# Kernel optimization log

Hardware: AMD Instinct MI355X
Metric: run time of the kernel (lower is better)

## Reference

```python
import jax, jax.numpy as jnp
import numpy as np

N = 16000      # points
K = 16         # neighbors per query (fixed-degree CSR)
M = N * K      # attention pairs
C = 384        # embed_dim
H = 6          # num_heads
HD = C // H    # head_dim = 64
L = 25         # quant_grid_length = window/quant = 6.0/0.24
T2 = 2 * L - 1 # rel-pos table length = 49
WIN = 6.0
QUANT = 0.24
SCALE = HD ** -0.5


def setup_inputs() -> dict:
    key = jax.random.key(0)
    ks = jax.random.split(key, 12)
    feats = jax.random.normal(ks[0], (N, C), jnp.float32)
    xyz = jax.random.uniform(ks[1], (N, 3), jnp.float32) * 240.0
    index_0 = jnp.repeat(jnp.arange(N, dtype=jnp.int32), K)            # sorted query ids per pair
    index_0_offsets = jnp.arange(0, M + 1, K, dtype=jnp.int32)         # CSR offsets
    index_1 = jax.random.randint(ks[2], (M,), 0, N, jnp.int32)         # key ids per pair
    sort_idx = jax.random.permutation(ks[3], N).astype(jnp.int32)
    lin = lambda k: jax.random.normal(k, (C, C), jnp.float32) * 0.02
    tab = lambda k: jax.random.normal(k, (T2, 3, H, HD), jnp.float32) * 0.02
    return {
        'feats': feats, 'xyz': xyz,
        'index_0': index_0, 'index_0_offsets': index_0_offsets,
        'index_1': index_1, 'sort_idx': sort_idx,
        'Wq': lin(ks[4]), 'bq': jnp.zeros((C,), jnp.float32),
        'Wk': lin(ks[5]), 'bk': jnp.zeros((C,), jnp.float32),
        'Wv': lin(ks[6]), 'bv': jnp.zeros((C,), jnp.float32),
        'Wp': lin(ks[7]), 'bp': jnp.zeros((C,), jnp.float32),
        'Tq': tab(ks[8]), 'Tk': tab(ks[9]), 'Tv': tab(ks[10]),
    }


def reference(feats, xyz, index_0, index_0_offsets, index_1, sort_idx,
              Wq, bq, Wk, bk, Wv, bv, Wp, bp, Tq, Tk, Tv):
    n = feats.shape[0]
    # QKV projections (key/value default to query feats in the module)
    q = (feats @ Wq.T + bq).reshape(n, H, HD) * SCALE
    k = (feats @ Wk.T + bk).reshape(n, H, HD)
    v = (feats @ Wv.T + bv).reshape(n, H, HD)
    # sort into contiguous-window order
    qs, ks_, vs = q[sort_idx], k[sort_idx], v[sort_idx]
    xyz_s = xyz[sort_idx]
    # quantized in-window coords (shift_win=False -> shift 0)
    xq = jnp.floor(((xyz_s - xyz_s.min(0)) % WIN) / QUANT)             # [N,3], values in [0, L-1]
    i0, i1 = index_0, index_1
    rel_idx = (xq[i0] - xq[i1]).astype(jnp.int32) + (L - 1)            # [M,3] in [0, 2L-2]
    # attention logits: q.k plus contextual relative-position terms
    attn = jnp.einsum('mhd,mhd->mh', qs[i0], ks_[i1])                  # [M,H]
    for t in range(3):
        dq = jnp.einsum('nhd,lhd->nlh', qs, Tq[:, t])                  # [N,T2,H]
        dk = jnp.einsum('nhd,lhd->nlh', ks_, Tk[:, t])
        attn = attn + dq[i0, rel_idx[:, t]] + dk[i1, rel_idx[:, t]]
    # scatter softmax over CSR segments (segments given by index_0)
    amax = jax.ops.segment_max(attn, i0, num_segments=n)
    e = jnp.exp(attn - amax[i0])
    denom = jax.ops.segment_sum(e, i0, num_segments=n)
    a = e / denom[i0]                                                  # [M,H]
    # weighted value aggregation
    x = jax.ops.segment_sum(a[:, :, None] * vs[i1], i0, num_segments=n)  # [N,H,HD]
    # relative-position value contribution, factored through table bins
    for t in range(3):
        seg2 = i0 * T2 + rel_idx[:, t]
        w = jax.ops.segment_sum(a, seg2, num_segments=n * T2).reshape(n, T2, H)
        x = x + jnp.einsum('nlh,lhd->nhd', w, Tv[:, t])
    # unsort back to input order and project
    out = jnp.zeros_like(x).at[sort_idx].set(x).reshape(n, C)
    return out @ Wp.T + bp
```

## Files before the change

### kernel.cpp

```cpp
#include <hip/hip_runtime.h>
#include <hip/hip_bf16.h>
#include <cstdint>
#include <cstddef>

#define NPTS 16000
#define KNB  16
#define CDIM 384
#define NH   6
#define HDIM 64
#define T2C  49
#define NL3T 147
#define THR  160
#define NXC  1152
#define ROWB 4224
#define QOFF  0
#define KOFF  768
#define VOFF  1536
#define DQOFF 2304
#define DKOFF 3264

static constexpr float WIN    = 6.0f;
static constexpr float QUANT  = 0.24f;
static constexpr float QSCALE = 0.125f;
static constexpr float DQS    = 8.0f;
static constexpr float DQSINV = 0.125f;

typedef __attribute__((ext_vector_type(8))) short short8;
typedef __attribute__((ext_vector_type(4))) float floatx4;
typedef __attribute__((ext_vector_type(4))) unsigned short ushort4v;

__device__ inline unsigned short f2bf(float x) {
    unsigned int u = __float_as_uint(x);
    unsigned int r = (u + 0x7fffu + ((u >> 16) & 1u)) >> 16;
    return (unsigned short)r;
}
__device__ inline float bf2f(unsigned short b) {
    return __uint_as_float(((unsigned int)b) << 16);
}
__device__ inline float f8tof(unsigned char b) {
    return __builtin_amdgcn_cvt_f32_fp8((int)b, 0);
}

__global__ void init_min_kernel(unsigned int* minbits) {
    if (threadIdx.x < 3) minbits[threadIdx.x] = 0x7f800000u;
}

__global__ void min_kernel(const float* __restrict__ xyz,
                           unsigned int* __restrict__ minbits) {
    float m0 = INFINITY, m1 = INFINITY, m2 = INFINITY;
    for (int i = blockIdx.x * blockDim.x + threadIdx.x; i < NPTS;
         i += gridDim.x * blockDim.x) {
        m0 = fminf(m0, xyz[i * 3 + 0]);
        m1 = fminf(m1, xyz[i * 3 + 1]);
        m2 = fminf(m2, xyz[i * 3 + 2]);
    }
#pragma unroll
    for (int off = 1; off < 64; off <<= 1) {
        m0 = fminf(m0, __shfl_xor(m0, off, 64));
        m1 = fminf(m1, __shfl_xor(m1, off, 64));
        m2 = fminf(m2, __shfl_xor(m2, off, 64));
    }
    if ((threadIdx.x & 63) == 0) {
        atomicMin(&minbits[0], __float_as_uint(m0));
        atomicMin(&minbits[1], __float_as_uint(m1));
        atomicMin(&minbits[2], __float_as_uint(m2));
    }
}

__global__ void xq_kernel(const float* __restrict__ xyz,
                          const int* __restrict__ sort_idx,
                          const unsigned int* __restrict__ minbits,
                          int* __restrict__ xq) {
    int n = blockIdx.x * blockDim.x + threadIdx.x;
    if (n >= NPTS) return;
    int orig = sort_idx[n];
#pragma unroll
    for (int t = 0; t < 3; ++t) {
        float mn = __uint_as_float(minbits[t]);
        float v  = xyz[orig * 3 + t] - mn;
        float md = fmodf(v, WIN);
        float q  = floorf(md / QUANT);
        xq[n * 3 + t] = (int)q;
    }
}

__global__ void relpack_kernel(const int* __restrict__ idx1,
                               const int* __restrict__ xq,
                               unsigned int* __restrict__ pairs) {
    int m = blockIdx.x * blockDim.x + threadIdx.x;
    if (m >= NPTS * KNB) return;
    int n = m >> 4;
    int key = idx1[m];
    int r0 = xq[n * 3 + 0] - xq[key * 3 + 0] + 24; r0 = min(max(r0, 0), T2C - 1);
    int r1 = xq[n * 3 + 1] - xq[key * 3 + 1] + 24; r1 = min(max(r1, 0), T2C - 1);
    int r2 = xq[n * 3 + 2] - xq[key * 3 + 2] + 24; r2 = min(max(r2, 0), T2C - 1);
    pairs[m] = (unsigned)key | ((unsigned)r0 << 14) | ((unsigned)r1 << 20) |
               ((unsigned)r2 << 26);
}

#define G0 (NPTS * CDIM / 4)
#define G1 (3 * CDIM * CDIM)
#define G2 (CDIM * CDIM)
#define G3 (NH * THR * HDIM)
#define G6 (NH * THR * HDIM)
#define G7 (NH * THR * HDIM)
#define G4 (3 * CDIM)
#define G5 (CDIM)
__global__ void prep_kernel(const float* __restrict__ feats,
                            const int* __restrict__ sortix,
                            const float* __restrict__ Wq,
                            const float* __restrict__ Wk,
                            const float* __restrict__ Wv,
                            const float* __restrict__ Wp,
                            const float* __restrict__ bq,
                            const float* __restrict__ bk,
                            const float* __restrict__ bv,
                            const float* __restrict__ bp,
                            const float* __restrict__ Tv,
                            const float* __restrict__ Tq,
                            const float* __restrict__ Tk,
                            unsigned short* __restrict__ featsbf,
                            unsigned short* __restrict__ Wall,
                            unsigned short* __restrict__ Wpbf,
                            unsigned short* __restrict__ Tvh,
                            unsigned short* __restrict__ Tqh,
                            unsigned short* __restrict__ Tkh,
                            float* __restrict__ bfull,
                            float* __restrict__ bproj) {
    int i = blockIdx.x * blockDim.x + threadIdx.x;
    if (i < G0) {
        int n  = i / (CDIM / 4);
        int c4 = (i % (CDIM / 4)) * 4;
        const float4 v = *(const float4*)&feats[(size_t)sortix[n] * CDIM + c4];
        ushort4v o;
        o.x = f2bf(v.x); o.y = f2bf(v.y); o.z = f2bf(v.z); o.w = f2bf(v.w);
        *(ushort4v*)&featsbf[(size_t)n * CDIM + c4] = o;
        return;
    }
    i -= G0;
    if (i < G1) {
        int j = i / CDIM, k = i % CDIM;
        float v = (j < 384) ? Wq[j * CDIM + k]
                : (j < 768) ? Wk[(j - 384) * CDIM + k]
                            : Wv[(j - 768) * CDIM + k];
        Wall[i] = f2bf(v);
        return;
    }
    i -= G1;
    if (i < G2) { Wpbf[i] = f2bf(Wp[i]); return; }
    i -= G2;
    if (i < G3) {
        int jr = (i / HDIM) % THR, d = i % HDIM, h = i / (THR * HDIM);
        Tvh[i] = (jr < NL3T) ? f2bf(Tv[(size_t)(jr * 6 + h) * HDIM + d])
                             : (unsigned short)0;
        return;
    }
    i -= G3;
    if (i < G6) {
        int jr = (i / HDIM) % THR, d = i % HDIM, h = i / (THR * HDIM);
        Tqh[i] = (jr < NL3T) ? f2bf(Tq[(size_t)(jr * 6 + h) * HDIM + d])
                             : (unsigned short)0;
        return;
    }
    i -= G6;
    if (i < G7) {
        int jr = (i / HDIM) % THR, d = i % HDIM, h = i / (THR * HDIM);
        Tkh[i] = (jr < NL3T) ? f2bf(Tk[(size_t)(jr * 6 + h) * HDIM + d])
                             : (unsigned short)0;
        return;
    }
    i -= G7;
    if (i < G4) {
        bfull[i] = (i < 384) ? bq[i] : (i < 768) ? bk[i - 384] : bv[i - 768];
        return;
    }
    i -= G4;
    if (i < G5) { bproj[i] = bp[i]; }
}

__global__ __launch_bounds__(256) void gemm_big(
    const unsigned short* __restrict__ Abf,
    const unsigned short* __restrict__ Wmat,
    const float* __restrict__ bias,
    int mode,
    unsigned char* __restrict__ QXb, float* __restrict__ outf) {
    __shared__ unsigned short As[128 * 64];
    __shared__ unsigned short Bs[128 * 64];
    const int tid  = threadIdx.x;
    const int lane = tid & 63;
    const int w    = tid >> 6;
    const int wm   = w >> 1, wn = w & 1;

    const int nwg  = gridDim.x * gridDim.y;
    const int orig = blockIdx.y * gridDim.x + blockIdx.x;
    const int qq   = nwg >> 3, rr = nwg & 7;
    const int xcd  = orig & 7, idx = orig >> 3;
    const int wg   = (xcd < rr ? xcd * (qq + 1) : rr * (qq + 1) + (xcd - rr) * qq) + idx;
    const int jn0  = (wg % gridDim.x) * 128;
    const int m0   = (wg / gridDim.x) * 128;

    floatx4 acc[4][4];
#pragma unroll
    for (int i = 0; i < 4; ++i)
#pragma unroll
        for (int j = 0; j < 4; ++j) acc[i][j] = (floatx4)0.0f;

    for (int kt = 0; kt < 6; ++kt) {
        const int k0 = kt * 64;
#pragma unroll
        for (int q = 0; q < 4; ++q) {
            const int s    = w * 4 + q;
            const int row  = s * 8 + (lane >> 3);
            const int col  = (lane & 7) * 8;
            const unsigned short* ga = Abf  + (size_t)(m0  + row) * CDIM + k0 + col;
            const unsigned short* gb = Wmat + (size_t)(jn0 + row) * CDIM + k0 + col;
            __builtin_amdgcn_global_load_lds(
                (const __attribute__((address_space(1))) void*)ga,
                (__attribute__((address_space(3))) void*)&As[s * 512], 16, 0, 0);
            __builtin_amdgcn_global_load_lds(
                (const __attribute__((address_space(1))) void*)gb,
                (__attribute__((address_space(3))) void*)&Bs[s * 512], 16, 0, 0);
        }
        __syncthreads();
#pragma unroll
        for (int ks = 0; ks < 2; ++ks) {
            short8 a[4], b[4];
#pragma unroll
            for (int mi = 0; mi < 4; ++mi) {
                int row = wm * 64 + mi * 16 + (lane & 15);
                a[mi] = *(const short8*)&As[row * 64 + ks * 32 + (lane >> 4) * 8];
            }
#pragma unroll
            for (int ni = 0; ni < 4; ++ni) {
                int jr = wn * 64 + ni * 16 + (lane & 15);
                b[ni] = *(const short8*)&Bs[jr * 64 + ks * 32 + (lane >> 4) * 8];
            }
#pragma unroll
            for (int mi = 0; mi < 4; ++mi)
#pragma unroll
                for (int ni = 0; ni < 4; ++ni)
                    acc[mi][ni] = __builtin_amdgcn_mfma_f32_16x16x32_bf16(
                        b[ni], a[mi], acc[mi][ni], 0, 0, 0);
        }
        __syncthreads();
    }

#pragma unroll
    for (int mi = 0; mi < 4; ++mi) {
        const int n = m0 + wm * 64 + mi * 16 + (lane & 15);
#pragma unroll
        for (int ni = 0; ni < 4; ++ni) {
            const int jjb = jn0 + wn * 64 + ni * 16 + (lane >> 4) * 4;
            const float4 b4 = *(const float4*)&bias[jjb];
            const float v0 = acc[mi][ni][0] + b4.x;
            const float v1 = acc[mi][ni][1] + b4.y;
            const float v2 = acc[mi][ni][2] + b4.z;
            const float v3 = acc[mi][ni][3] + b4.w;
            if (mode == 0) {
                const float scl = (jjb < 384) ? QSCALE : 1.0f;
                ushort4v o;
                o.x = f2bf(v0 * scl); o.y = f2bf(v1 * scl);
                o.z = f2bf(v2 * scl); o.w = f2bf(v3 * scl);
                *(ushort4v*)(QXb + (size_t)n * ROWB + jjb * 2) = o;
            } else {
                float4 o; o.x = v0; o.y = v1; o.z = v2; o.w = v3;
                *(float4*)&outf[(size_t)n * CDIM + jjb] = o;
            }
        }
    }
}

__global__ __launch_bounds__(256) void dqdk_kernel(
    const unsigned char* __restrict__ QXin,
    const unsigned short* __restrict__ Tqh,
    const unsigned short* __restrict__ Tkh,
    unsigned char* __restrict__ QXout) {
    __shared__ unsigned short As[128 * 64];
    __shared__ unsigned short Bs[THR * 64];
    const int tid  = threadIdx.x;
    const int lane = tid & 63;
    const int w    = tid >> 6;
    const int wm   = w >> 1, wn = w & 1;
    const int h    = blockIdx.y;
    const bool isk = blockIdx.z != 0;
    const int srcoff = (isk ? KOFF : QOFF) + h * 128;
    const int dstoff = (isk ? DKOFF : DQOFF) + h * THR;
    const unsigned short* T = (isk ? Tkh : Tqh) + (size_t)h * THR * HDIM;
    const int m0 = blockIdx.x * 128;

#pragma unroll
    for (int q = 0; q < 4; ++q) {
        const int s   = w * 4 + q;
        const int row = s * 8 + (lane >> 3);
        const unsigned char* ga =
            QXin + (size_t)(m0 + row) * ROWB + srcoff + (lane & 7) * 16;
        __builtin_amdgcn_global_load_lds(
            (const __attribute__((address_space(1))) void*)ga,
            (__attribute__((address_space(3))) void*)&As[s * 512], 16, 0, 0);
    }
#pragma unroll
    for (int q = 0; q < 5; ++q) {
        const int s   = w * 5 + q;
        const int row = s * 8 + (lane >> 3);
        const unsigned short* gb = T + (size_t)row * HDIM + (lane & 7) * 8;
        __builtin_amdgcn_global_load_lds(
            (const __attribute__((address_space(1))) void*)gb,
            (__attribute__((address_space(3))) void*)&Bs[s * 512], 16, 0, 0);
    }
    __syncthreads();

    floatx4 acc[4][5];
#pragma unroll
    for (int i = 0; i < 4; ++i)
#pragma unroll
        for (int j = 0; j < 5; ++j) acc[i][j] = (floatx4)0.0f;

#pragma unroll
    for (int ks = 0; ks < 2; ++ks) {
        short8 a[4], b[5];
#pragma unroll
        for (int mi = 0; mi < 4; ++mi) {
            int row = wm * 64 + mi * 16 + (lane & 15);
            a[mi] = *(const short8*)&As[row * 64 + ks * 32 + (lane >> 4) * 8];
        }
#pragma unroll
        for (int ni = 0; ni < 5; ++ni) {
            int jr = wn * 80 + ni * 16 + (lane & 15);
            b[ni] = *(const short8*)&Bs[jr * 64 + ks * 32 + (lane >> 4) * 8];
        }
#pragma unroll
        for (int mi = 0; mi < 4; ++mi)
#pragma unroll
            for (int ni = 0; ni < 5; ++ni)
                acc[mi][ni] = __builtin_amdgcn_mfma_f32_16x16x32_bf16(
                    b[ni], a[mi], acc[mi][ni], 0, 0, 0);
    }

#pragma unroll
    for (int mi = 0; mi < 4; ++mi) {
        const int n = m0 + wm * 64 + mi * 16 + (lane & 15);
#pragma unroll
        for (int ni = 0; ni < 5; ++ni) {
            const int jr0 = wn * 80 + ni * 16 + (lane >> 4) * 4;
            int u = __builtin_amdgcn_cvt_pk_fp8_f32(acc[mi][ni][0] * DQS,
                                                    acc[mi][ni][1] * DQS, 0, false);
            u = __builtin_amdgcn_cvt_pk_fp8_f32(acc[mi][ni][2] * DQS,
                                                acc[mi][ni][3] * DQS, u, true);
            *(unsigned int*)(QXout + (size_t)n * ROWB + dstoff + jr0) = (unsigned)u;
        }
    }
}

__global__ __launch_bounds__(384) void attn_kernel(
    const unsigned char* __restrict__ QXb,
    const unsigned int* __restrict__ pairs,
    const unsigned short* __restrict__ Tvh,
    const int* __restrict__ sortix,
    unsigned short* __restrict__ xb) {
    const int n    = blockIdx.x;
    const int h    = threadIdx.x >> 6;
    const int lane = threadIdx.x & 63;
    const int pp   = lane >> 4, c = lane & 15;
    const int hb   = h * THR;
    const unsigned short* Tvb = Tvh + (size_t)hb * HDIM;

    const unsigned char* qrow = QXb + (size_t)n * ROWB;
    const ushort4v q4 = *(const ushort4v*)(qrow + QOFF + h * 128 + c * 8);
    const float qx = bf2f(q4.x), qy = bf2f(q4.y), qz = bf2f(q4.z), qw = bf2f(q4.w);

    unsigned int pv[4];
#pragma unroll
    for (int g = 0; g < 4; ++g) pv[g] = pairs[n * KNB + g * 4 + pp];

    const unsigned char* krow[4];
    int j0g[4], j1g[4], j2g[4];
#pragma unroll
    for (int g = 0; g < 4; ++g) {
        krow[g] = QXb + (size_t)(pv[g] & 0x3FFFu) * ROWB;
        j0g[g]  = (int)((pv[g] >> 14) & 63u) * 3;
        j1g[g]  = (int)((pv[g] >> 20) & 63u) * 3 + 1;
        j2g[g]  = (int)(pv[g] >> 26) * 3 + 2;
    }

    float tab[4];
#pragma unroll
    for (int g = 0; g < 4; ++g) {
        tab[g] = DQSINV *
            (f8tof(qrow[DQOFF + hb + j0g[g]]) + f8tof(qrow[DQOFF + hb + j1g[g]]) +
             f8tof(qrow[DQOFF + hb + j2g[g]]) +
             f8tof(krow[g][DKOFF + hb + j0g[g]]) +
             f8tof(krow[g][DKOFF + hb + j1g[g]]) +
             f8tof(krow[g][DKOFF + hb + j2g[g]]));
    }

    float lg[4];
#pragma unroll
    for (int g = 0; g < 4; ++g) {
        const ushort4v k4 = *(const ushort4v*)(krow[g] + KOFF + h * 128 + c * 8);
        lg[g] = qx * bf2f(k4.x) + qy * bf2f(k4.y) + qz * bf2f(k4.z) + qw * bf2f(k4.w);
    }
#pragma unroll
    for (int m = 1; m <= 8; m <<= 1)
#pragma unroll
        for (int g = 0; g < 4; ++g) lg[g] += __shfl_xor(lg[g], m, 64);
#pragma unroll
    for (int g = 0; g < 4; ++g) lg[g] += tab[g];

    float mx = fmaxf(fmaxf(lg[0], lg[1]), fmaxf(lg[2], lg[3]));
    mx = fmaxf(mx, __shfl_xor(mx, 16, 64));
    mx = fmaxf(mx, __shfl_xor(mx, 32, 64));
    float e[4], s = 0.f;
#pragma unroll
    for (int g = 0; g < 4; ++g) { e[g] = expf(lg[g] - mx); s += e[g]; }
    s += __shfl_xor(s, 16, 64);
    s += __shfl_xor(s, 32, 64);
    const float inv = 1.f / s;

    float xa0 = 0.f, xa1 = 0.f, xa2 = 0.f, xa3 = 0.f;
#pragma unroll
    for (int g = 0; g < 4; ++g) {
        const float wgt = e[g] * inv;
        const ushort4v v4 = *(const ushort4v*)(krow[g] + VOFF + h * 128 + c * 8);
        const ushort4v t0 = *(const ushort4v*)&Tvb[(size_t)j0g[g] * HDIM + c * 4];
        const ushort4v t1 = *(const ushort4v*)&Tvb[(size_t)j1g[g] * HDIM + c * 4];
        const ushort4v t2 = *(const ushort4v*)&Tvb[(size_t)j2g[g] * HDIM + c * 4];
        xa0 += wgt * (bf2f(v4.x) + bf2f(t0.x) + bf2f(t1.x) + bf2f(t2.x));
        xa1 += wgt * (bf2f(v4.y) + bf2f(t0.y) + bf2f(t1.y) + bf2f(t2.y));
        xa2 += wgt * (bf2f(v4.z) + bf2f(t0.z) + bf2f(t1.z) + bf2f(t2.z));
        xa3 += wgt * (bf2f(v4.w) + bf2f(t0.w) + bf2f(t1.w) + bf2f(t2.w));
    }
#pragma unroll
    for (int m = 16; m <= 32; m <<= 1) {
        xa0 += __shfl_xor(xa0, m, 64);
        xa1 += __shfl_xor(xa1, m, 64);
        xa2 += __shfl_xor(xa2, m, 64);
        xa3 += __shfl_xor(xa3, m, 64);
    }
    if (pp == 0) {
        const int dst = sortix[n];
        ushort4v o;
        o.x = f2bf(xa0); o.y = f2bf(xa1); o.z = f2bf(xa2); o.w = f2bf(xa3);
        *(ushort4v*)&xb[(size_t)dst * CDIM + h * HDIM + c * 4] = o;
    }
}

extern "C" void kernel_launch(void* const* d_in, const int* in_sizes, int n_in,
                              void* d_out, int out_size, void* d_ws,
                              size_t ws_size, hipStream_t stream) {
    const float* feats  = (const float*)d_in[0];
    const float* xyz    = (const float*)d_in[1];
    const int*   index1 = (const int*)d_in[4];
    const int*   sortix = (const int*)d_in[5];
    const float* Wq = (const float*)d_in[6];
    const float* bq = (const float*)d_in[7];
    const float* Wk = (const float*)d_in[8];
    const float* bk = (const float*)d_in[9];
    const float* Wv = (const float*)d_in[10];
    const float* bv = (const float*)d_in[11];
    const float* Wp = (const float*)d_in[12];
    const float* bp = (const float*)d_in[13];
    const float* Tq = (const float*)d_in[14];
    const float* Tk = (const float*)d_in[15];
    const float* Tv = (const float*)d_in[16];
    float* out = (float*)d_out;

    char* ws = (char*)d_ws;
    size_t off = 0;
    auto alloc = [&](size_t bytes) -> void* {
        void* p = ws + off;
        off = (off + bytes + 255) & ~(size_t)255;
        return p;
    };
    unsigned short* featsbf = (unsigned short*)alloc((size_t)NPTS * CDIM * 2);
    unsigned short* Wall    = (unsigned short*)alloc((size_t)NXC * CDIM * 2);
    unsigned short* Wpbf    = (unsigned short*)alloc((size_t)CDIM * CDIM * 2);
    unsigned short* Tvh     = (unsigned short*)alloc((size_t)NH * THR * HDIM * 2);
    unsigned short* Tqh     = (unsigned short*)alloc((size_t)NH * THR * HDIM * 2);
    unsigned short* Tkh     = (unsigned short*)alloc((size_t)NH * THR * HDIM * 2);
    float*          bfull   = (float*)alloc((size_t)NXC * sizeof(float));
    float*          bproj   = (float*)alloc((size_t)CDIM * sizeof(float));
    unsigned char*  QXb     = (unsigned char*)alloc((size_t)NPTS * ROWB);
    unsigned int*   pairs   = (unsigned int*)alloc((size_t)NPTS * KNB * 4);
    int*            xq      = (int*)alloc((size_t)NPTS * 3 * sizeof(int));
    unsigned int*   minbits = (unsigned int*)alloc(16);
    unsigned short* xb      = featsbf;

    init_min_kernel<<<1, 64, 0, stream>>>(minbits);
    min_kernel<<<128, 256, 0, stream>>>(xyz, minbits);
    xq_kernel<<<(NPTS + 255) / 256, 256, 0, stream>>>(xyz, sortix, minbits, xq);
    relpack_kernel<<<(NPTS * KNB + 255) / 256, 256, 0, stream>>>(index1, xq, pairs);

    const int prep_total = G0 + G1 + G2 + G3 + G6 + G7 + G4 + G5;
    prep_kernel<<<(prep_total + 255) / 256, 256, 0, stream>>>(
        feats, sortix, Wq, Wk, Wv, Wp, bq, bk, bv, bp, Tv, Tq, Tk,
        featsbf, Wall, Wpbf, Tvh, Tqh, Tkh, bfull, bproj);

    dim3 g0(NXC / 128, NPTS / 128);
    gemm_big<<<g0, 256, 0, stream>>>(featsbf, Wall, bfull, 0, QXb,
                                     (float*)nullptr);

    dim3 gd(NPTS / 128, NH, 2);
    dqdk_kernel<<<gd, 256, 0, stream>>>(QXb, Tqh, Tkh, QXb);

    attn_kernel<<<NPTS, 384, 0, stream>>>(QXb, pairs, Tvh, sortix, xb);

    dim3 g1(CDIM / 128, NPTS / 128);
    gemm_big<<<g1, 256, 0, stream>>>(xb, Wpbf, bproj, 1, (unsigned char*)nullptr,
                                     out);
}
```

Measured before the change: 218.5 us.

## Split QKV buffer into head-major planes and precompute relative-position logits separately

Measured after the change: 207.3 us. 5.1% less time.

```diff
diff --git a/kernel.cpp b/kernel.cpp
--- a/kernel.cpp
+++ b/kernel.cpp
@@ -12,12 +12,6 @@
 #define NL3T 147
 #define THR  160
 #define NXC  1152
-#define ROWB 4224
-#define QOFF  0
-#define KOFF  768
-#define VOFF  1536
-#define DQOFF 2304
-#define DKOFF 3264
 
 static constexpr float WIN    = 6.0f;
 static constexpr float QUANT  = 0.24f;
@@ -39,6 +33,17 @@
 }
 __device__ inline float f8tof(unsigned char b) {
     return __builtin_amdgcn_cvt_f32_fp8((int)b, 0);
+}
+
+__device__ inline void swz_nh(int& nb, int& h) {
+    const int gx   = gridDim.x;
+    const int nwg  = gx * NH;
+    const int orig = blockIdx.y * gx + blockIdx.x;
+    const int q    = nwg >> 3, r = nwg & 7;
+    const int xcd  = orig & 7, idx = orig >> 3;
+    const int wg   = (xcd < r ? xcd * (q + 1) : r * (q + 1) + (xcd - r) * q) + idx;
+    h  = wg / gx;
+    nb = wg % gx;
 }
 
 __global__ void init_min_kernel(unsigned int* minbits) {
@@ -183,7 +188,8 @@
     const unsigned short* __restrict__ Wmat,
     const float* __restrict__ bias,
     int mode,
-    unsigned char* __restrict__ QXb, float* __restrict__ outf) {
+    unsigned char* __restrict__ qh8, unsigned char* __restrict__ kvh8,
+    float* __restrict__ outf) {
     __shared__ unsigned short As[128 * 64];
     __shared__ unsigned short Bs[128 * 64];
     const int tid  = threadIdx.x;
@@ -257,11 +263,21 @@
             const float v2 = acc[mi][ni][2] + b4.z;
             const float v3 = acc[mi][ni][3] + b4.w;
             if (mode == 0) {
-                const float scl = (jjb < 384) ? QSCALE : 1.0f;
-                ushort4v o;
-                o.x = f2bf(v0 * scl); o.y = f2bf(v1 * scl);
-                o.z = f2bf(v2 * scl); o.w = f2bf(v3 * scl);
-                *(ushort4v*)(QXb + (size_t)n * ROWB + jjb * 2) = o;
+                if (jjb < 384) {
+                    const int h = jjb >> 6, d = jjb & 63;
+                    ushort4v o;
+                    o.x = f2bf(v0 * QSCALE); o.y = f2bf(v1 * QSCALE);
+                    o.z = f2bf(v2 * QSCALE); o.w = f2bf(v3 * QSCALE);
+                    *(ushort4v*)(qh8 + ((size_t)h * NPTS + n) * 128 + d * 2) = o;
+                } else {
+                    const int jj = (jjb < 768) ? jjb - 384 : jjb - 768;
+                    const int h = jj >> 6, d = jj & 63;
+                    const int slot = (jjb < 768) ? 0 : 128;
+                    ushort4v o;
+                    o.x = f2bf(v0); o.y = f2bf(v1);
+                    o.z = f2bf(v2); o.w = f2bf(v3);
+                    *(ushort4v*)(kvh8 + ((size_t)h * NPTS + n) * 256 + slot + d * 2) = o;
+                }
             } else {
                 float4 o; o.x = v0; o.y = v1; o.z = v2; o.w = v3;
                 *(float4*)&outf[(size_t)n * CDIM + jjb] = o;
@@ -271,10 +287,12 @@
 }
 
 __global__ __launch_bounds__(256) void dqdk_kernel(
-    const unsigned char* __restrict__ QXin,
+    const unsigned char* __restrict__ qh8,
+    const unsigned char* __restrict__ kvh8,
     const unsigned short* __restrict__ Tqh,
     const unsigned short* __restrict__ Tkh,
-    unsigned char* __restrict__ QXout) {
+    unsigned char* __restrict__ dqh,
+    unsigned char* __restrict__ dkh) {
     __shared__ unsigned short As[128 * 64];
     __shared__ unsigned short Bs[THR * 64];
     const int tid  = threadIdx.x;
@@ -283,8 +301,10 @@
     const int wm   = w >> 1, wn = w & 1;
     const int h    = blockIdx.y;
     const bool isk = blockIdx.z != 0;
-    const int srcoff = (isk ? KOFF : QOFF) + h * 128;
-    const int dstoff = (isk ? DKOFF : DQOFF) + h * THR;
+    const unsigned char* srcb = isk ? kvh8 + (size_t)h * NPTS * 256
+                                    : qh8  + (size_t)h * NPTS * 128;
+    const int sstride = isk ? 256 : 128;
+    unsigned char* dst = (isk ? dkh : dqh) + (size_t)h * NPTS * THR;
     const unsigned short* T = (isk ? Tkh : Tqh) + (size_t)h * THR * HDIM;
     const int m0 = blockIdx.x * 128;
 
@@ -292,8 +312,7 @@
     for (int q = 0; q < 4; ++q) {
         const int s   = w * 4 + q;
         const int row = s * 8 + (lane >> 3);
-        const unsigned char* ga =
-            QXin + (size_t)(m0 + row) * ROWB + srcoff + (lane & 7) * 16;
+        const unsigned char* ga = srcb + (size_t)(m0 + row) * sstride + (lane & 7) * 16;
         __builtin_amdgcn_global_load_lds(
             (const __attribute__((address_space(1))) void*)ga,
             (__attribute__((address_space(3))) void*)&As[s * 512], 16, 0, 0);
@@ -346,26 +365,57 @@
                                                     acc[mi][ni][1] * DQS, 0, false);
             u = __builtin_amdgcn_cvt_pk_fp8_f32(acc[mi][ni][2] * DQS,
                                                 acc[mi][ni][3] * DQS, u, true);
-            *(unsigned int*)(QXout + (size_t)n * ROWB + dstoff + jr0) = (unsigned)u;
+            *(unsigned int*)(dst + (size_t)n * THR + jr0) = (unsigned)u;
         }
     }
 }
 
-__global__ __launch_bounds__(384) void attn_kernel(
-    const unsigned char* __restrict__ QXb,
+__global__ __launch_bounds__(256) void tqk_kernel(
     const unsigned int* __restrict__ pairs,
+    const unsigned char* __restrict__ dqh,
+    const unsigned char* __restrict__ dkh,
+    unsigned short* __restrict__ tqk) {
+    int nb, h;
+    swz_nh(nb, h);
+    const int n = nb * 4 + (threadIdx.x >> 6);
+    const int lane = threadIdx.x & 63;
+    const int p = lane >> 2, s = lane & 3;
+
+    const unsigned int pv = pairs[n * KNB + p];
+    float v = 0.0f;
+    if (s < 3) {
+        const int key = (int)(pv & 0x3FFFu);
+        const int r = (int)((pv >> (14 + 6 * s)) & 63u);
+        const int jr = r * 3 + s;
+        v = f8tof(dqh[(size_t)h * NPTS * THR + (size_t)n * THR + jr]) +
+            f8tof(dkh[(size_t)h * NPTS * THR + (size_t)key * THR + jr]);
+    }
+    v += __shfl_xor(v, 1, 64);
+    v += __shfl_xor(v, 2, 64);
+    if (s == 0)
+        tqk[((size_t)h * NPTS + n) * KNB + p] = f2bf(v * DQSINV);
+}
+
+__global__ __launch_bounds__(256) void attn_kernel(
+    const unsigned char* __restrict__ qh8,
+    const unsigned char* __restrict__ kvh8,
+    const unsigned int* __restrict__ pairs,
+    const unsigned short* __restrict__ tqk,
     const unsigned short* __restrict__ Tvh,
     const int* __restrict__ sortix,
     unsigned short* __restrict__ xb) {
-    const int n    = blockIdx.x;
-    const int h    = threadIdx.x >> 6;
+    int nb, h;
+    swz_nh(nb, h);
+    const int n = nb * 4 + (threadIdx.x >> 6);
     const int lane = threadIdx.x & 63;
-    const int pp   = lane >> 4, c = lane & 15;
-    const int hb   = h * THR;
-    const unsigned short* Tvb = Tvh + (size_t)hb * HDIM;
-
-    const unsigned char* qrow = QXb + (size_t)n * ROWB;
-    const ushort4v q4 = *(const ushort4v*)(qrow + QOFF + h * 128 + c * 8);
+    const int pp = lane >> 4, c = lane & 15;
+
+    const unsigned char* kvb = kvh8 + (size_t)h * NPTS * 256;
+    const unsigned short* Tvb = Tvh + (size_t)h * THR * HDIM;
+    const unsigned short* tqr = tqk + ((size_t)h * NPTS + n) * KNB;
+
+    const ushort4v q4 =
+        *(const ushort4v*)(qh8 + ((size_t)h * NPTS + n) * 128 + c * 8);
     const float qx = bf2f(q4.x), qy = bf2f(q4.y), qz = bf2f(q4.z), qw = bf2f(q4.w);
 
     unsigned int pv[4];
@@ -376,27 +426,16 @@
     int j0g[4], j1g[4], j2g[4];
 #pragma unroll
     for (int g = 0; g < 4; ++g) {
-        krow[g] = QXb + (size_t)(pv[g] & 0x3FFFu) * ROWB;
+        krow[g] = kvb + (size_t)(pv[g] & 0x3FFFu) * 256;
         j0g[g]  = (int)((pv[g] >> 14) & 63u) * 3;
         j1g[g]  = (int)((pv[g] >> 20) & 63u) * 3 + 1;
         j2g[g]  = (int)(pv[g] >> 26) * 3 + 2;
     }
 
-    float tab[4];
+    float lg[4];
 #pragma unroll
     for (int g = 0; g < 4; ++g) {
-        tab[g] = DQSINV *
-            (f8tof(qrow[DQOFF + hb + j0g[g]]) + f8tof(qrow[DQOFF + hb + j1g[g]]) +
-             f8tof(qrow[DQOFF + hb + j2g[g]]) +
-             f8tof(krow[g][DKOFF + hb + j0g[g]]) +
-             f8tof(krow[g][DKOFF + hb + j1g[g]]) +
-             f8tof(krow[g][DKOFF + hb + j2g[g]]));
-    }
-
-    float lg[4];
-#pragma unroll
-    for (int g = 0; g < 4; ++g) {
-        const ushort4v k4 = *(const ushort4v*)(krow[g] + KOFF + h * 128 + c * 8);
+        const ushort4v k4 = *(const ushort4v*)(krow[g] + c * 8);
         lg[g] = qx * bf2f(k4.x) + qy * bf2f(k4.y) + qz * bf2f(k4.z) + qw * bf2f(k4.w);
     }
 #pragma unroll
@@ -404,7 +443,7 @@
 #pragma unroll
         for (int g = 0; g < 4; ++g) lg[g] += __shfl_xor(lg[g], m, 64);
 #pragma unroll
-    for (int g = 0; g < 4; ++g) lg[g] += tab[g];
+    for (int g = 0; g < 4; ++g) lg[g] += bf2f(tqr[g * 4 + pp]);
 
     float mx = fmaxf(fmaxf(lg[0], lg[1]), fmaxf(lg[2], lg[3]));
     mx = fmaxf(mx, __shfl_xor(mx, 16, 64));
@@ -420,7 +459,7 @@
 #pragma unroll
     for (int g = 0; g < 4; ++g) {
         const float wgt = e[g] * inv;
-        const ushort4v v4 = *(const ushort4v*)(krow[g] + VOFF + h * 128 + c * 8);
+        const ushort4v v4 = *(const ushort4v*)(krow[g] + 128 + c * 8);
         const ushort4v t0 = *(const ushort4v*)&Tvb[(size_t)j0g[g] * HDIM + c * 4];
         const ushort4v t1 = *(const ushort4v*)&Tvb[(size_t)j1g[g] * HDIM + c * 4];
         const ushort4v t2 = *(const ushort4v*)&Tvb[(size_t)j2g[g] * HDIM + c * 4];
@@ -479,7 +518,11 @@
     unsigned short* Tkh     = (unsigned short*)alloc((size_t)NH * THR * HDIM * 2);
     float*          bfull   = (float*)alloc((size_t)NXC * sizeof(float));
     float*          bproj   = (float*)alloc((size_t)CDIM * sizeof(float));
-    unsigned char*  QXb     = (unsigned char*)alloc((size_t)NPTS * ROWB);
+    unsigned char*  qh8     = (unsigned char*)alloc((size_t)NH * NPTS * 128);
+    unsigned char*  kvh8    = (unsigned char*)alloc((size_t)NH * NPTS * 256);
+    unsigned char*  dqh     = (unsigned char*)alloc((size_t)NH * NPTS * THR);
+    unsigned char*  dkh     = (unsigned char*)alloc((size_t)NH * NPTS * THR);
+    unsigned short* tqk     = (unsigned short*)alloc((size_t)NH * NPTS * KNB * 2);
     unsigned int*   pairs   = (unsigned int*)alloc((size_t)NPTS * KNB * 4);
     int*            xq      = (int*)alloc((size_t)NPTS * 3 * sizeof(int));
     unsigned int*   minbits = (unsigned int*)alloc(16);
@@ -496,15 +539,18 @@
         featsbf, Wall, Wpbf, Tvh, Tqh, Tkh, bfull, bproj);
 
     dim3 g0(NXC / 128, NPTS / 128);
-    gemm_big<<<g0, 256, 0, stream>>>(featsbf, Wall, bfull, 0, QXb,
+    gemm_big<<<g0, 256, 0, stream>>>(featsbf, Wall, bfull, 0, qh8, kvh8,
                                      (float*)nullptr);
 
     dim3 gd(NPTS / 128, NH, 2);
-    dqdk_kernel<<<gd, 256, 0, stream>>>(QXb, Tqh, Tkh, QXb);
-
-    attn_kernel<<<NPTS, 384, 0, stream>>>(QXb, pairs, Tvh, sortix, xb);
+    dqdk_kernel<<<gd, 256, 0, stream>>>(qh8, kvh8, Tqh, Tkh, dqh, dkh);
+
+    dim3 ga(NPTS / 4, NH);
+    tqk_kernel<<<ga, 256, 0, stream>>>(pairs, dqh, dkh, tqk);
+
+    attn_kernel<<<ga, 256, 0, stream>>>(qh8, kvh8, pairs, tqk, Tvh, sortix, xb);
 
     dim3 g1(CDIM / 128, NPTS / 128);
     gemm_big<<<g1, 256, 0, stream>>>(xb, Wpbf, bproj, 1, (unsigned char*)nullptr,
-                                     out);
-}
+                                     (unsigned char*)nullptr, out);
+}
```
